# Kernel optimization log

Hardware: AMD Instinct MI355X
Metric: run time of the kernel (lower is better)

Reference implementation:

```python
import jax, jax.numpy as jnp
import numpy as np

N_TYPES = 10000   # len(fs.inodes)
HID = 256         # fs.size
BATCH = 32
SEQ = 1024


def _build_tree(rng):
    # random recursive tree: parent[i] uniform in [0, i), root parent = -1
    parent = np.full(N_TYPES, -1, np.int64)
    parent[1:] = (rng.random(N_TYPES - 1) * np.arange(1, N_TYPES)).astype(np.int64)
    # depth (number of nodes on root path incl. self)
    depth = np.ones(N_TYPES, np.int64)
    for i in range(1, N_TYPES):
        depth[i] = depth[parent[i]] + 1
    D = int(depth.max())
    # ancestor table: anc[n, d] = d-th ancestor of n (anc[n,0]=n), -1 padding
    anc = np.full((N_TYPES, D), -1, np.int32)
    anc[:, 0] = np.arange(N_TYPES)
    cur = parent.copy()
    for d in range(1, D):
        anc[:, d] = cur
        cur = np.where(cur >= 0, parent[np.maximum(cur, 0)], -1)
    return anc


def setup_inputs() -> dict:
    key = jax.random.key(0)
    ks = jax.random.split(key, 8)
    rng = np.random.default_rng(0)
    anc = jnp.asarray(_build_tree(rng))  # [N, D] int32
    k = 1.0 / np.sqrt(HID)
    inp = {
        "event_seqs": jax.random.randint(ks[0], (BATCH, SEQ), 0, N_TYPES),
        "anc": anc,
        "weight": jax.random.uniform(ks[1], (N_TYPES,), jnp.float32, -0.1, 0.1),
        "emb": jax.random.normal(ks[2], (N_TYPES, HID), jnp.float32),
        "W_ih": jax.random.uniform(ks[3], (4 * HID, HID), jnp.float32, -k, k),
        "W_hh": jax.random.uniform(ks[4], (4 * HID, HID), jnp.float32, -k, k),
        "b_ih": jax.random.uniform(ks[5], (4 * HID,), jnp.float32, -k, k),
        "b_hh": jax.random.uniform(ks[6], (4 * HID,), jnp.float32, -k, k),
    }
    return inp


def _path_table(anc, weight, emb):
    # path[n] = sum_d (prod_{j<d} weight[anc[n,j]]) * emb[anc[n,d]], over valid ancestors
    valid = anc >= 0                                  # [N, D]
    anc_safe = jnp.where(valid, anc, 0)
    w = jnp.where(valid, weight[anc_safe], 1.0)       # [N, D]
    cumw = jnp.cumprod(w, axis=1)
    cumw = jnp.concatenate([jnp.ones_like(cumw[:, :1]), cumw[:, :-1]], axis=1)
    cumw = jnp.where(valid, cumw, 0.0)
    e = emb[anc_safe]                                 # [N, D, H]
    return jnp.einsum("nd,ndh->nh", cumw, e)          # [N, H]


def _lstm(emb_seq, W_ih, W_hh, b_ih, b_hh):
    # emb_seq: [T, B, H]; torch LSTM gate order i, f, g, o
    H = W_hh.shape[1]
    B = emb_seq.shape[1]
    x_proj = jnp.einsum("tbh,gh->tbg", emb_seq, W_ih) + b_ih + b_hh  # [T, B, 4H]

    def step(carry, x_t):
        h, c = carry
        gates = x_t + h @ W_hh.T
        i, f, g, o = jnp.split(gates, 4, axis=-1)
        i, f, o = jax.nn.sigmoid(i), jax.nn.sigmoid(f), jax.nn.sigmoid(o)
        g = jnp.tanh(g)
        c = f * c + i * g
        h = o * jnp.tanh(c)
        return (h, c), h

    h0 = jnp.zeros((B, H), emb_seq.dtype)
    (hn, cn), out = jax.lax.scan(step, (h0, h0), x_proj)
    return out, hn, cn


def reference(event_seqs, anc, weight, emb, W_ih, W_hh, b_ih, b_hh):
    path = _path_table(anc, weight, emb)       # [N, H]
    emb_seq = path[event_seqs.T]               # [T, B, H] (torch transposes to seq-first)
    out, hn, cn = _lstm(emb_seq, W_ih, W_hh, b_ih, b_hh)
    return out
```

## Files before the change

### kernel.cpp

```cpp
#include <hip/hip_runtime.h>

typedef unsigned int uint;
typedef unsigned long long u64;
typedef unsigned short ushort;
typedef _Float16 f16;
typedef _Float16 f16x2 __attribute__((ext_vector_type(2)));
typedef _Float16 f16x8 __attribute__((ext_vector_type(8)));
typedef float f32x4 __attribute__((ext_vector_type(4)));

#define N_TYPES 10000
#define HID 256
#define G4 1024
#define BATCH 32
#define SEQ 1024

__global__ void k_path(const int* __restrict__ anc, const float* __restrict__ weight,
                       const float* __restrict__ emb, int D, f16* __restrict__ path) {
  int n = blockIdx.x;
  int h = threadIdx.x;
  float acc = 0.f, cw = 1.f;
  for (int d = 0; d < D; ++d) {
    int a = anc[n * D + d];
    if (a < 0) break;
    acc += cw * emb[a * HID + h];
    cw *= weight[a];
  }
  path[n * HID + h] = (f16)acc;
}

__global__ void k_conv(const float* __restrict__ wih, const float* __restrict__ whh,
                       const float* __restrict__ bih, const float* __restrict__ bhh,
                       f16* __restrict__ wih_h, uint* __restrict__ whh_t,
                       float* __restrict__ bias) {
  int i = blockIdx.x * 256 + threadIdx.x;
  wih_h[i] = (f16)wih[i];
  if (i < G4 * 128) {
    int row = i >> 7, p = i & 127;
    f16x2 v;
    v.x = (f16)whh[row * HID + 2 * p];
    v.y = (f16)whh[row * HID + 2 * p + 1];
    whh_t[p * G4 + row] = __builtin_bit_cast(uint, v);
  }
  if (i < G4) bias[i] = bih[i] + bhh[i];
}

#define BM 128
#define BN 128
#define BK 64
#define LPAD 72
__global__ __launch_bounds__(256) void k_gemm(const f16* __restrict__ A,
                                              const f16* __restrict__ Bw,
                                              const float* __restrict__ bias,
                                              f16* __restrict__ C) {
  __shared__ f16 sA[BM][LPAD];
  __shared__ f16 sB[BN][LPAD];
  int m0 = blockIdx.x * BM, n0 = blockIdx.y * BN;
  int tid = threadIdx.x;
  int wid = tid >> 6, lane = tid & 63;
  int wm = wid & 1, wn = wid >> 1;
  f32x4 acc[4][4] = {};
  for (int k0 = 0; k0 < 256; k0 += BK) {
    __syncthreads();
    int r = tid >> 3, kc = (tid & 7) * 8;
    for (int i = 0; i < 4; ++i) {
      int row = r + 32 * i;
      int gm = m0 + row;
      uint4 va = make_uint4(0u, 0u, 0u, 0u);
      if (gm < N_TYPES) va = *(const uint4*)&A[gm * 256 + k0 + kc];
      *(uint4*)&sA[row][kc] = va;
      uint4 vb = *(const uint4*)&Bw[(n0 + row) * 256 + k0 + kc];
      *(uint4*)&sB[row][kc] = vb;
    }
    __syncthreads();
#pragma unroll
    for (int ks = 0; ks < 2; ++ks) {
      f16x8 af[4], bf[4];
      int kk = ks * 32 + (lane >> 4) * 8;
#pragma unroll
      for (int mt = 0; mt < 4; ++mt)
        af[mt] = *(const f16x8*)&sA[wm * 64 + mt * 16 + (lane & 15)][kk];
#pragma unroll
      for (int nt = 0; nt < 4; ++nt)
        bf[nt] = *(const f16x8*)&sB[wn * 64 + nt * 16 + (lane & 15)][kk];
#pragma unroll
      for (int mt = 0; mt < 4; ++mt)
#pragma unroll
        for (int nt = 0; nt < 4; ++nt)
          acc[mt][nt] = __builtin_amdgcn_mfma_f32_16x16x32_f16(af[mt], bf[nt], acc[mt][nt], 0, 0, 0);
    }
  }
#pragma unroll
  for (int mt = 0; mt < 4; ++mt)
#pragma unroll
    for (int nt = 0; nt < 4; ++nt)
#pragma unroll
      for (int qq = 0; qq < 4; ++qq) {
        int row = m0 + wm * 64 + mt * 16 + (lane >> 4) * 4 + qq;
        int col = n0 + wn * 64 + nt * 16 + (lane & 15);
        int dim = col & 255, g = col >> 8;
        if (row < N_TYPES)
          C[row * G4 + dim * 4 + g] = (f16)(acc[mt][nt][qq] + bias[col]);
      }
}

__device__ __forceinline__ float dot2(uint wp, uint hp, float acc) {
#if __has_builtin(__builtin_amdgcn_fdot2)
  return __builtin_amdgcn_fdot2(__builtin_bit_cast(f16x2, wp),
                                __builtin_bit_cast(f16x2, hp), acc, false);
#else
  f16x2 a = __builtin_bit_cast(f16x2, wp);
  f16x2 b = __builtin_bit_cast(f16x2, hp);
  return acc + (float)a.x * (float)b.x + (float)a.y * (float)b.y;
#endif
}

__device__ __forceinline__ float sigm(float v) { return 1.f / (1.f + __expf(-v)); }
__device__ __forceinline__ float tanh_(float v) { return 1.f - 2.f / (__expf(2.f * v) + 1.f); }
__device__ __forceinline__ float f16u(ushort u) { return (float)__builtin_bit_cast(f16, u); }

__global__ __launch_bounds__(512)
__attribute__((amdgpu_waves_per_eu(2, 2)))
void k_lstm(const int* __restrict__ evs,
            const f16* __restrict__ proj,
            const uint* __restrict__ whh_t,
            u64* hglob,
            float* __restrict__ out) {
  int bid = blockIdx.x;
  int b = bid & 31, q = bid >> 5;
  int t = threadIdx.x;
  int v = t >> 6, l = t & 63;
  int kq = v >> 1;
  int rid = (v & 1) * 64 + l;
  int rowg = (rid >> 5) * 256 + q * 32 + (rid & 31);

  __shared__ float pl[2][4][128];

  uint w[32];
#pragma unroll
  for (int i = 0; i < 32; ++i) w[i] = whh_t[(kq * 32 + i) * G4 + rowg];

  u64* hb = hglob + b * 256;
  const int* ev = evs + b * SEQ;

  float x0 = 0.f, x1 = 0.f, x2 = 0.f, x3 = 0.f;
  if (t < 32) {
    ushort4 xv = *(const ushort4*)(proj + (long)ev[0] * G4 + (q * 32 + t) * 4);
    x0 = f16u(xv.x); x1 = f16u(xv.y); x2 = f16u(xv.z); x3 = f16u(xv.w);
  }

  float c = 0.f;

  for (int step = 0; step < SEQ; ++step) {
    int h0 = 0;
    if (step > 0 && l >= 32) {
      const u64* src = hb + ((step - 1) & 1) * 128 + kq * 32 + (l - 32);
      u64 val;
      do {
        val = __hip_atomic_load(src, __ATOMIC_RELAXED, __HIP_MEMORY_SCOPE_AGENT);
      } while ((uint)(val >> 32) != (uint)step);
      h0 = (int)(uint)val;
    }

    float a0 = 0.f, a1 = 0.f, a2 = 0.f, a3 = 0.f;
#pragma unroll
    for (int i = 0; i < 32; i += 4) {
      a0 = dot2(w[i + 0], (uint)__builtin_amdgcn_readlane(h0, 32 + i + 0), a0);
      a1 = dot2(w[i + 1], (uint)__builtin_amdgcn_readlane(h0, 32 + i + 1), a1);
      a2 = dot2(w[i + 2], (uint)__builtin_amdgcn_readlane(h0, 32 + i + 2), a2);
      a3 = dot2(w[i + 3], (uint)__builtin_amdgcn_readlane(h0, 32 + i + 3), a3);
    }
    pl[step & 1][kq][rid] = (a0 + a1) + (a2 + a3);

    __syncthreads();

    if (t < 32) {
      const float (*pp)[128] = pl[step & 1];
      float s0 = (pp[0][t]      + pp[1][t])      + (pp[2][t]      + pp[3][t])      + x0;
      float s1 = (pp[0][32 + t] + pp[1][32 + t]) + (pp[2][32 + t] + pp[3][32 + t]) + x1;
      float s2 = (pp[0][64 + t] + pp[1][64 + t]) + (pp[2][64 + t] + pp[3][64 + t]) + x2;
      float s3 = (pp[0][96 + t] + pp[1][96 + t]) + (pp[2][96 + t] + pp[3][96 + t]) + x3;
      float iv = sigm(s0), fv = sigm(s1), gv = tanh_(s2), ov = sigm(s3);
      c = fv * c + iv * gv;
      float hval = ov * tanh_(c);
      float hA = __shfl(hval, 2 * (t & 15));
      float hB = __shfl(hval, 2 * (t & 15) + 1);
      if (t < 16) {
        f16x2 pk; pk.x = (f16)hA; pk.y = (f16)hB;
        uint pku = __builtin_bit_cast(uint, pk);
        u64 val = (u64)pku | ((u64)(uint)(step + 1) << 32);
        __hip_atomic_store(hb + (step & 1) * 128 + q * 16 + t, val,
                           __ATOMIC_RELAXED, __HIP_MEMORY_SCOPE_AGENT);
      }
      out[(step * BATCH + b) * HID + q * 32 + t] = hval;
      if (step + 1 < SEQ) {
        ushort4 xv = *(const ushort4*)(proj + (long)ev[step + 1] * G4 + (q * 32 + t) * 4);
        x0 = f16u(xv.x); x1 = f16u(xv.y); x2 = f16u(xv.z); x3 = f16u(xv.w);
      }
    }
  }
}

extern "C" void kernel_launch(void* const* d_in, const int* in_sizes, int n_in,
                              void* d_out, int out_size, void* d_ws, size_t ws_size,
                              hipStream_t stream) {
  (void)n_in; (void)out_size; (void)ws_size;
  const int* evs = (const int*)d_in[0];
  const int* anc = (const int*)d_in[1];
  const float* weight = (const float*)d_in[2];
  const float* emb = (const float*)d_in[3];
  const float* wih = (const float*)d_in[4];
  const float* whh = (const float*)d_in[5];
  const float* bih = (const float*)d_in[6];
  const float* bhh = (const float*)d_in[7];
  int D = in_sizes[1] / N_TYPES;

  char* ws = (char*)d_ws;
  f16* path = (f16*)(ws);
  f16* wih_h = (f16*)(ws + 5242880);
  uint* whh_t = (uint*)(ws + 5767168);
  float* bias = (float*)(ws + 6291456);
  f16* proj = (f16*)(ws + 6295552);
  u64* hglob = (u64*)(ws + 26775552);
  float* out = (float*)d_out;

  k_conv<<<1024, 256, 0, stream>>>(wih, whh, bih, bhh, wih_h, whh_t, bias);
  k_path<<<N_TYPES, 256, 0, stream>>>(anc, weight, emb, D, path);
  k_gemm<<<dim3(79, 8), 256, 0, stream>>>(path, wih_h, bias, proj);
  hipMemsetAsync(hglob, 0, 32 * 2 * 128 * 8, stream);
  k_lstm<<<256, 512, 0, stream>>>(evs, proj, whh_t, hglob, out);
}
```

Baseline: 1.603 ms.

## Run each batch LSTM in a single block with W_hh in registers and LDS

The recurrent LSTM is restructured from 256 blocks, eight per batch element, that exchanged hidden state through global atomics and spin-waits into 32 blocks, one per batch element. Each block keeps the whole W_hh slice in registers (100 packed pairs per row) plus LDS (the remaining 28), and exchanges h through shared memory using only __syncthreads. This removes cross-block global polling latency each step. In exchange each block does 8x more dot work per step on far fewer CUs, and the large register arrays risk spills with waves_per_eu fixed at 2.

New measurement: 2.450 ms. +52.8%, slower.

```diff
diff --git a/kernel.cpp b/kernel.cpp
--- a/kernel.cpp
+++ b/kernel.cpp
@@ -1,7 +1,6 @@
 #include <hip/hip_runtime.h>
 
 typedef unsigned int uint;
-typedef unsigned long long u64;
 typedef unsigned short ushort;
 typedef _Float16 f16;
 typedef _Float16 f16x2 __attribute__((ext_vector_type(2)));
@@ -13,6 +12,8 @@
 #define G4 1024
 #define BATCH 32
 #define SEQ 1024
+#define NV 100
+#define NL 7
 
 __global__ void k_path(const int* __restrict__ anc, const float* __restrict__ weight,
                        const float* __restrict__ emb, int D, f16* __restrict__ path) {
@@ -123,81 +124,103 @@
 void k_lstm(const int* __restrict__ evs,
             const f16* __restrict__ proj,
             const uint* __restrict__ whh_t,
-            u64* hglob,
             float* __restrict__ out) {
-  int bid = blockIdx.x;
-  int b = bid & 31, q = bid >> 5;
+  int b = blockIdx.x;
   int t = threadIdx.x;
-  int v = t >> 6, l = t & 63;
-  int kq = v >> 1;
-  int rid = (v & 1) * 64 + l;
-  int rowg = (rid >> 5) * 256 + q * 32 + (rid & 31);
-
-  __shared__ float pl[2][4][128];
-
-  uint w[32];
-#pragma unroll
-  for (int i = 0; i < 32; ++i) w[i] = whh_t[(kq * 32 + i) * G4 + rowg];
-
-  u64* hb = hglob + b * 256;
+
+  __shared__ uint4 wlds4[NL][1024];
+  __shared__ float sl[1024];
+  __shared__ uint hl[128];
+
+#pragma unroll
+  for (int g = 0; g < NL; ++g) {
+    int p = NV + 4 * g;
+    uint4 a;
+    a.x = whh_t[(p + 0) * G4 + t];
+    a.y = whh_t[(p + 1) * G4 + t];
+    a.z = whh_t[(p + 2) * G4 + t];
+    a.w = whh_t[(p + 3) * G4 + t];
+    wlds4[g][t] = a;
+    uint4 bb;
+    bb.x = whh_t[(p + 0) * G4 + 512 + t];
+    bb.y = whh_t[(p + 1) * G4 + 512 + t];
+    bb.z = whh_t[(p + 2) * G4 + 512 + t];
+    bb.w = whh_t[(p + 3) * G4 + 512 + t];
+    wlds4[g][512 + t] = bb;
+  }
+
+  uint w0[NV], w1[NV];
+#pragma unroll
+  for (int p = 0; p < NV; ++p) {
+    w0[p] = whh_t[p * G4 + t];
+    w1[p] = whh_t[p * G4 + 512 + t];
+  }
+
   const int* ev = evs + b * SEQ;
-
-  float x0 = 0.f, x1 = 0.f, x2 = 0.f, x3 = 0.f;
-  if (t < 32) {
-    ushort4 xv = *(const ushort4*)(proj + (long)ev[0] * G4 + (q * 32 + t) * 4);
-    x0 = f16u(xv.x); x1 = f16u(xv.y); x2 = f16u(xv.z); x3 = f16u(xv.w);
-  }
-
-  float c = 0.f;
+  float c = 0.f, hval_prev = 0.f;
+
+  __syncthreads();
 
   for (int step = 0; step < SEQ; ++step) {
-    int h0 = 0;
-    if (step > 0 && l >= 32) {
-      const u64* src = hb + ((step - 1) & 1) * 128 + kq * 32 + (l - 32);
-      u64 val;
-      do {
-        val = __hip_atomic_load(src, __ATOMIC_RELAXED, __HIP_MEMORY_SCOPE_AGENT);
-      } while ((uint)(val >> 32) != (uint)step);
-      h0 = (int)(uint)val;
-    }
-
-    float a0 = 0.f, a1 = 0.f, a2 = 0.f, a3 = 0.f;
-#pragma unroll
-    for (int i = 0; i < 32; i += 4) {
-      a0 = dot2(w[i + 0], (uint)__builtin_amdgcn_readlane(h0, 32 + i + 0), a0);
-      a1 = dot2(w[i + 1], (uint)__builtin_amdgcn_readlane(h0, 32 + i + 1), a1);
-      a2 = dot2(w[i + 2], (uint)__builtin_amdgcn_readlane(h0, 32 + i + 2), a2);
-      a3 = dot2(w[i + 3], (uint)__builtin_amdgcn_readlane(h0, 32 + i + 3), a3);
-    }
-    pl[step & 1][kq][rid] = (a0 + a1) + (a2 + a3);
-
-    __syncthreads();
-
-    if (t < 32) {
-      const float (*pp)[128] = pl[step & 1];
-      float s0 = (pp[0][t]      + pp[1][t])      + (pp[2][t]      + pp[3][t])      + x0;
-      float s1 = (pp[0][32 + t] + pp[1][32 + t]) + (pp[2][32 + t] + pp[3][32 + t]) + x1;
-      float s2 = (pp[0][64 + t] + pp[1][64 + t]) + (pp[2][64 + t] + pp[3][64 + t]) + x2;
-      float s3 = (pp[0][96 + t] + pp[1][96 + t]) + (pp[2][96 + t] + pp[3][96 + t]) + x3;
+    float x0 = 0.f, x1 = 0.f, x2 = 0.f, x3 = 0.f;
+    if (t < 256) {
+      if (step > 0) out[((step - 1) * BATCH + b) * HID + t] = hval_prev;
+      ushort4 xv = *(const ushort4*)(proj + (long)ev[step] * G4 + t * 4);
+      x0 = f16u(xv.x); x1 = f16u(xv.y); x2 = f16u(xv.z); x3 = f16u(xv.w);
+    }
+
+    float a0 = 0.f, a1 = 0.f;
+    if (step > 0) {
+      const uint4* hl4 = (const uint4*)hl;
+#pragma unroll
+      for (int i = 0; i < NV / 4; ++i) {
+        uint4 h4 = hl4[i];
+        a0 = dot2(w0[4 * i + 0], h4.x, a0);
+        a0 = dot2(w0[4 * i + 1], h4.y, a0);
+        a0 = dot2(w0[4 * i + 2], h4.z, a0);
+        a0 = dot2(w0[4 * i + 3], h4.w, a0);
+        a1 = dot2(w1[4 * i + 0], h4.x, a1);
+        a1 = dot2(w1[4 * i + 1], h4.y, a1);
+        a1 = dot2(w1[4 * i + 2], h4.z, a1);
+        a1 = dot2(w1[4 * i + 3], h4.w, a1);
+      }
+#pragma unroll
+      for (int g = 0; g < NL; ++g) {
+        uint4 h4 = hl4[NV / 4 + g];
+        uint4 v0 = wlds4[g][t];
+        uint4 v1 = wlds4[g][512 + t];
+        a0 = dot2(v0.x, h4.x, a0);
+        a0 = dot2(v0.y, h4.y, a0);
+        a0 = dot2(v0.z, h4.z, a0);
+        a0 = dot2(v0.w, h4.w, a0);
+        a1 = dot2(v1.x, h4.x, a1);
+        a1 = dot2(v1.y, h4.y, a1);
+        a1 = dot2(v1.z, h4.z, a1);
+        a1 = dot2(v1.w, h4.w, a1);
+      }
+    }
+    sl[t] = a0;
+    sl[512 + t] = a1;
+    __syncthreads();
+
+    if (t < 256) {
+      float s0 = sl[t]       + x0;
+      float s1 = sl[256 + t] + x1;
+      float s2 = sl[512 + t] + x2;
+      float s3 = sl[768 + t] + x3;
       float iv = sigm(s0), fv = sigm(s1), gv = tanh_(s2), ov = sigm(s3);
       c = fv * c + iv * gv;
       float hval = ov * tanh_(c);
-      float hA = __shfl(hval, 2 * (t & 15));
-      float hB = __shfl(hval, 2 * (t & 15) + 1);
-      if (t < 16) {
-        f16x2 pk; pk.x = (f16)hA; pk.y = (f16)hB;
-        uint pku = __builtin_bit_cast(uint, pk);
-        u64 val = (u64)pku | ((u64)(uint)(step + 1) << 32);
-        __hip_atomic_store(hb + (step & 1) * 128 + q * 16 + t, val,
-                           __ATOMIC_RELAXED, __HIP_MEMORY_SCOPE_AGENT);
-      }
-      out[(step * BATCH + b) * HID + q * 32 + t] = hval;
-      if (step + 1 < SEQ) {
-        ushort4 xv = *(const ushort4*)(proj + (long)ev[step + 1] * G4 + (q * 32 + t) * 4);
-        x0 = f16u(xv.x); x1 = f16u(xv.y); x2 = f16u(xv.z); x3 = f16u(xv.w);
-      }
-    }
-  }
+      hval_prev = hval;
+      float hn = __shfl_down(hval, 1);
+      if ((t & 1) == 0) {
+        f16x2 pk; pk.x = (f16)hval; pk.y = (f16)hn;
+        hl[t >> 1] = __builtin_bit_cast(uint, pk);
+      }
+    }
+    __syncthreads();
+  }
+  if (t < 256) out[((SEQ - 1) * BATCH + b) * HID + t] = hval_prev;
 }
 
 extern "C" void kernel_launch(void* const* d_in, const int* in_sizes, int n_in,
@@ -220,12 +243,10 @@
   uint* whh_t = (uint*)(ws + 5767168);
   float* bias = (float*)(ws + 6291456);
   f16* proj = (f16*)(ws + 6295552);
-  u64* hglob = (u64*)(ws + 26775552);
   float* out = (float*)d_out;
 
   k_conv<<<1024, 256, 0, stream>>>(wih, whh, bih, bhh, wih_h, whh_t, bias);
   k_path<<<N_TYPES, 256, 0, stream>>>(anc, weight, emb, D, path);
   k_gemm<<<dim3(79, 8), 256, 0, stream>>>(path, wih_h, bias, proj);
-  hipMemsetAsync(hglob, 0, 32 * 2 * 128 * 8, stream);
-  k_lstm<<<256, 512, 0, stream>>>(evs, proj, whh_t, hglob, out);
-}
+  k_lstm<<<32, 512, 0, stream>>>(evs, proj, whh_t, out);
+}
```
